# Kernel optimization log

Hardware: AMD Instinct MI355X
Metric: run time of the kernel (lower is better)

Reference implementation:

```python
import jax, jax.numpy as jnp
import numpy as np

VOCAB = 100000
DIM = 256
BATCH = 16384
CTX = 20          # 2 * context_window
NUM_NEG = 5
ALPHA = 0.5
EPS = 1e-6


def setup_inputs() -> dict:
    key = jax.random.key(0)
    k_t, k_c, k_n, k_f, k_wf, k_wr, k_wi = jax.random.split(key, 7)
    # xavier_uniform bound for [VOCAB, DIM] weight
    bound = float(np.sqrt(6.0 / (VOCAB + DIM)))
    return {
        "target_tokens": jax.random.randint(k_t, (BATCH,), 0, VOCAB),
        "context_tokens": jax.random.randint(k_c, (BATCH, CTX), 0, VOCAB),
        "negative_samples": jax.random.randint(k_n, (BATCH, NUM_NEG), 0, VOCAB),
        "token_frequencies": jax.random.uniform(k_f, (VOCAB,), jnp.float32, 1.0, 1000.0),
        "W_fwd": jax.random.uniform(k_wf, (VOCAB, DIM), jnp.float32, -bound, bound),
        "W_rev": jax.random.uniform(k_wr, (VOCAB, DIM), jnp.float32, -bound, bound),
        "W_iso": jax.random.normal(k_wi, (VOCAB, DIM), jnp.float32) * 0.02,
    }


def reference(target_tokens, context_tokens, negative_samples,
              token_frequencies, W_fwd, W_rev, W_iso):
    # blended (orphic) embedding per target token: [B, D]
    contextual = ALPHA * W_fwd[target_tokens] + (1.0 - ALPHA) * W_rev[target_tokens]
    scaling = 1.0 / (1.0 + jnp.log(token_frequencies + EPS))          # [V]
    orphic = contextual + W_iso[target_tokens] * scaling[target_tokens][:, None]

    # positive skip-gram scores: [B, C]
    pos_scores = jnp.einsum('bd,bcd->bc', orphic, W_fwd[context_tokens])
    positive_loss = -jnp.log(jax.nn.sigmoid(pos_scores) + EPS).mean()

    # negative scores: [B, K]; per-sample mean, summed over batch (matches torch loop)
    neg_scores = jnp.einsum('bd,bkd->bk', orphic, W_fwd[negative_samples])
    negative_loss = (-jnp.log(jax.nn.sigmoid(-neg_scores) + EPS)).mean(axis=1).sum()

    return positive_loss + negative_loss
```

## Files before the change

### kernel.cpp

```cpp
#include <hip/hip_runtime.h>
#include <hip/hip_fp8.h>
#include <math.h>

#define VOCAB   100000
#define DIM     256
#define BATCH   16384
#define CTX     20
#define NUM_NEG 5
#define NTOK    (CTX + NUM_NEG)
#define ALPHA   0.5f
#define EPS     1e-6f
#define SCALE     512.0f
#define INV_SCALE (1.0f / 512.0f)

#define WAVES_PER_BLOCK 4
#define NBLOCKS (BATCH / WAVES_PER_BLOCK)

#if __has_builtin(__builtin_amdgcn_cvt_pk_f32_fp8) && __has_builtin(__builtin_amdgcn_cvt_pk_fp8_f32)
#define HW_FP8 1
typedef float v2f __attribute__((ext_vector_type(2)));
#else
#define HW_FP8 0
#endif

__global__ __launch_bounds__(256) void convert_wf(
    const float* __restrict__ Wf, uint4* __restrict__ wf8)
{
    const size_t t = (size_t)blockIdx.x * 256 + threadIdx.x;
    const float4* src = (const float4*)Wf + t * 4;
    float4 a = src[0], b = src[1], c = src[2], d = src[3];
    unsigned int r0, r1, r2, r3;
#if HW_FP8
    r0 = (unsigned)__builtin_amdgcn_cvt_pk_fp8_f32(a.x*SCALE, a.y*SCALE, 0, false);
    r0 = (unsigned)__builtin_amdgcn_cvt_pk_fp8_f32(a.z*SCALE, a.w*SCALE, (int)r0, true);
    r1 = (unsigned)__builtin_amdgcn_cvt_pk_fp8_f32(b.x*SCALE, b.y*SCALE, 0, false);
    r1 = (unsigned)__builtin_amdgcn_cvt_pk_fp8_f32(b.z*SCALE, b.w*SCALE, (int)r1, true);
    r2 = (unsigned)__builtin_amdgcn_cvt_pk_fp8_f32(c.x*SCALE, c.y*SCALE, 0, false);
    r2 = (unsigned)__builtin_amdgcn_cvt_pk_fp8_f32(c.z*SCALE, c.w*SCALE, (int)r2, true);
    r3 = (unsigned)__builtin_amdgcn_cvt_pk_fp8_f32(d.x*SCALE, d.y*SCALE, 0, false);
    r3 = (unsigned)__builtin_amdgcn_cvt_pk_fp8_f32(d.z*SCALE, d.w*SCALE, (int)r3, true);
#else
    {
        const float v[16] = {a.x,a.y,a.z,a.w,b.x,b.y,b.z,b.w,c.x,c.y,c.z,c.w,d.x,d.y,d.z,d.w};
        unsigned int rr[4] = {0,0,0,0};
        for (int i = 0; i < 16; ++i) {
            unsigned int byte = (unsigned int)__hip_cvt_float_to_fp8(v[i]*SCALE, __HIP_SATFINITE, __HIP_E4M3);
            rr[i >> 2] |= byte << ((i & 3) * 8);
        }
        r0 = rr[0]; r1 = rr[1]; r2 = rr[2]; r3 = rr[3];
    }
#endif
    wf8[t] = make_uint4(r0, r1, r2, r3);
}

__device__ __forceinline__ void decode8(unsigned int u, float* e) {
#if HW_FP8
    v2f p0 = __builtin_amdgcn_cvt_pk_f32_fp8((int)u, false);
    v2f p1 = __builtin_amdgcn_cvt_pk_f32_fp8((int)u, true);
    e[0] = p0.x; e[1] = p0.y; e[2] = p1.x; e[3] = p1.y;
#else
    for (int i = 0; i < 4; ++i) {
        __half_raw h = __hip_cvt_fp8_to_halfraw((__hip_fp8_storage_t)((u >> (8*i)) & 0xFF), __HIP_E4M3);
        e[i] = __half2float(__half(h));
    }
#endif
}

__global__ __launch_bounds__(256) void orphic_main_fp8(
    const int*   __restrict__ tgt,
    const int*   __restrict__ ctx,
    const int*   __restrict__ neg,
    const float* __restrict__ freq,
    const float* __restrict__ Wf,
    const float* __restrict__ Wr,
    const float* __restrict__ Wi,
    const uint4* __restrict__ wf8,
    float*       __restrict__ partial)
{
    const int wave = threadIdx.x >> 6;
    const int lane = threadIdx.x & 63;
    const int g    = lane >> 4;
    const int q    = lane & 15;
    const int b    = blockIdx.x * WAVES_PER_BLOCK + wave;

    const int t = tgt[b];
    const float* ft  = Wf + (size_t)t * DIM + q * 16;
    const float* rt  = Wr + (size_t)t * DIM + q * 16;
    const float* it_ = Wi + (size_t)t * DIM + q * 16;
    float o[16];
    {
        float4 f0 = *(const float4*)(ft + 0),  f1 = *(const float4*)(ft + 4);
        float4 f2 = *(const float4*)(ft + 8),  f3 = *(const float4*)(ft + 12);
        float4 r0 = *(const float4*)(rt + 0),  r1 = *(const float4*)(rt + 4);
        float4 r2 = *(const float4*)(rt + 8),  r3 = *(const float4*)(rt + 12);
        float4 w0 = *(const float4*)(it_ + 0), w1 = *(const float4*)(it_ + 4);
        float4 w2 = *(const float4*)(it_ + 8), w3 = *(const float4*)(it_ + 12);
        const float sc = 1.0f / (1.0f + logf(freq[t] + EPS));
        const float ff[16] = {f0.x,f0.y,f0.z,f0.w,f1.x,f1.y,f1.z,f1.w,f2.x,f2.y,f2.z,f2.w,f3.x,f3.y,f3.z,f3.w};
        const float rr[16] = {r0.x,r0.y,r0.z,r0.w,r1.x,r1.y,r1.z,r1.w,r2.x,r2.y,r2.z,r2.w,r3.x,r3.y,r3.z,r3.w};
        const float ww[16] = {w0.x,w0.y,w0.z,w0.w,w1.x,w1.y,w1.z,w1.w,w2.x,w2.y,w2.z,w2.w,w3.x,w3.y,w3.z,w3.w};
        #pragma unroll
        for (int i = 0; i < 16; ++i)
            o[i] = ALPHA * ff[i] + (1.0f - ALPHA) * rr[i] + ww[i] * sc;
    }

    int tok = 0;
    if (lane < CTX)       tok = ctx[(size_t)b * CTX + lane];
    else if (lane < NTOK) tok = neg[(size_t)b * NUM_NEG + (lane - CTX)];

    float posacc = 0.0f, negacc = 0.0f;

    #pragma unroll 2
    for (int it = 0; it < 7; ++it) {
        const int j = it * 4 + g;
        const bool valid = (j < NTOK);
        const int jc = valid ? j : (NTOK - 1);
        const int tj = __shfl(tok, jc, 64);

        const uint4 u = wf8[(size_t)tj * (DIM / 16) + q];
        float e[16];
        decode8(u.x, e + 0);
        decode8(u.y, e + 4);
        decode8(u.z, e + 8);
        decode8(u.w, e + 12);

        float d = 0.0f;
        #pragma unroll
        for (int i = 0; i < 16; ++i) d += o[i] * e[i];

        d += __shfl_xor(d, 1, 64);
        d += __shfl_xor(d, 2, 64);
        d += __shfl_xor(d, 4, 64);
        d += __shfl_xor(d, 8, 64);

        const float s = d * INV_SCALE;
        const float sgn = (jc < CTX) ? -1.0f : 1.0f;
        const float loss = -logf(1.0f / (1.0f + expf(sgn * s)) + EPS);
        if (valid) {
            if (jc < CTX) posacc += loss;
            else          negacc += loss;
        }
    }
    negacc *= (1.0f / NUM_NEG);

    float p = (q == 0) ? posacc : 0.0f;
    float n = (q == 0) ? negacc : 0.0f;
    p += __shfl_xor(p, 16, 64);  p += __shfl_xor(p, 32, 64);
    n += __shfl_xor(n, 16, 64);  n += __shfl_xor(n, 32, 64);

    __shared__ float sp[WAVES_PER_BLOCK];
    __shared__ float sn[WAVES_PER_BLOCK];
    if (lane == 0) { sp[wave] = p; sn[wave] = n; }
    __syncthreads();
    if (threadIdx.x == 0) {
        partial[(size_t)blockIdx.x * 2 + 0] = sp[0] + sp[1] + sp[2] + sp[3];
        partial[(size_t)blockIdx.x * 2 + 1] = sn[0] + sn[1] + sn[2] + sn[3];
    }
}

__global__ __launch_bounds__(256) void orphic_main_f32(
    const int*   __restrict__ tgt,
    const int*   __restrict__ ctx,
    const int*   __restrict__ neg,
    const float* __restrict__ freq,
    const float* __restrict__ Wf,
    const float* __restrict__ Wr,
    const float* __restrict__ Wi,
    float*       __restrict__ partial)
{
    const int wave = threadIdx.x >> 6;
    const int lane = threadIdx.x & 63;
    const int g    = lane >> 4;
    const int q    = lane & 15;
    const int b    = blockIdx.x * WAVES_PER_BLOCK + wave;

    const int t = tgt[b];
    const float* ft  = Wf + (size_t)t * DIM + q * 16;
    const float* rt  = Wr + (size_t)t * DIM + q * 16;
    const float* it_ = Wi + (size_t)t * DIM + q * 16;
    float o[16];
    {
        const float sc = 1.0f / (1.0f + logf(freq[t] + EPS));
        #pragma unroll
        for (int i = 0; i < 16; ++i)
            o[i] = ALPHA * ft[i] + (1.0f - ALPHA) * rt[i] + it_[i] * sc;
    }

    int tok = 0;
    if (lane < CTX)       tok = ctx[(size_t)b * CTX + lane];
    else if (lane < NTOK) tok = neg[(size_t)b * NUM_NEG + (lane - CTX)];

    float posacc = 0.0f, negacc = 0.0f;
    #pragma unroll 2
    for (int it = 0; it < 7; ++it) {
        const int j = it * 4 + g;
        const bool valid = (j < NTOK);
        const int jc = valid ? j : (NTOK - 1);
        const int tj = __shfl(tok, jc, 64);
        const float* e = Wf + (size_t)tj * DIM + q * 16;
        float d = 0.0f;
        #pragma unroll
        for (int i = 0; i < 16; ++i) d += o[i] * e[i];
        d += __shfl_xor(d, 1, 64);
        d += __shfl_xor(d, 2, 64);
        d += __shfl_xor(d, 4, 64);
        d += __shfl_xor(d, 8, 64);
        const float sgn = (jc < CTX) ? -1.0f : 1.0f;
        const float loss = -logf(1.0f / (1.0f + expf(sgn * d)) + EPS);
        if (valid) {
            if (jc < CTX) posacc += loss;
            else          negacc += loss;
        }
    }
    negacc *= (1.0f / NUM_NEG);

    float p = (q == 0) ? posacc : 0.0f;
    float n = (q == 0) ? negacc : 0.0f;
    p += __shfl_xor(p, 16, 64);  p += __shfl_xor(p, 32, 64);
    n += __shfl_xor(n, 16, 64);  n += __shfl_xor(n, 32, 64);

    __shared__ float sp[WAVES_PER_BLOCK];
    __shared__ float sn[WAVES_PER_BLOCK];
    if (lane == 0) { sp[wave] = p; sn[wave] = n; }
    __syncthreads();
    if (threadIdx.x == 0) {
        partial[(size_t)blockIdx.x * 2 + 0] = sp[0] + sp[1] + sp[2] + sp[3];
        partial[(size_t)blockIdx.x * 2 + 1] = sn[0] + sn[1] + sn[2] + sn[3];
    }
}

__global__ __launch_bounds__(256) void orphic_reduce(
    const float* __restrict__ partial, float* __restrict__ out)
{
    double p = 0.0, n = 0.0;
    for (int i = threadIdx.x; i < NBLOCKS; i += 256) {
        p += (double)partial[(size_t)i * 2 + 0];
        n += (double)partial[(size_t)i * 2 + 1];
    }
    __shared__ double lp[256];
    __shared__ double ln[256];
    lp[threadIdx.x] = p;
    ln[threadIdx.x] = n;
    __syncthreads();
    for (int s = 128; s > 0; s >>= 1) {
        if (threadIdx.x < s) {
            lp[threadIdx.x] += lp[threadIdx.x + s];
            ln[threadIdx.x] += ln[threadIdx.x + s];
        }
        __syncthreads();
    }
    if (threadIdx.x == 0) {
        out[0] = (float)(lp[0] / (double)((size_t)BATCH * CTX) + ln[0]);
    }
}

extern "C" void kernel_launch(void* const* d_in, const int* in_sizes, int n_in,
                              void* d_out, int out_size, void* d_ws, size_t ws_size,
                              hipStream_t stream) {
    const int*   tgt  = (const int*)  d_in[0];
    const int*   ctx  = (const int*)  d_in[1];
    const int*   neg  = (const int*)  d_in[2];
    const float* freq = (const float*)d_in[3];
    const float* Wf   = (const float*)d_in[4];
    const float* Wr   = (const float*)d_in[5];
    const float* Wi   = (const float*)d_in[6];
    float* out = (float*)d_out;

    const size_t tbl_bytes = (size_t)VOCAB * DIM;
    const size_t need = tbl_bytes + (size_t)NBLOCKS * 2 * sizeof(float);

    if (ws_size >= need) {
        uint4* wf8 = (uint4*)d_ws;
        float* partial = (float*)((char*)d_ws + tbl_bytes);
        convert_wf<<<VOCAB * DIM / 16 / 256, 256, 0, stream>>>(Wf, wf8);
        orphic_main_fp8<<<NBLOCKS, 256, 0, stream>>>(tgt, ctx, neg, freq, Wf, Wr, Wi, wf8, partial);
        orphic_reduce<<<1, 256, 0, stream>>>(partial, out);
    } else {
        float* partial = (float*)d_ws;
        orphic_main_f32<<<NBLOCKS, 256, 0, stream>>>(tgt, ctx, neg, freq, Wf, Wr, Wi, partial);
        orphic_reduce<<<1, 256, 0, stream>>>(partial, out);
    }
}
```

Before: 53.02 us.

## Merge fp8 table conversion with orphic-row build and batch gather loads in scorer

The fp8 conversion of W_fwd and the computation of the blended orphic rows now run as two block ranges of a single kernel, so the orphic gathers from three fp32 tables overlap with the table conversion. The scoring kernel reads precomputed orphic rows and issues all seven fp8 gathers up front before decoding, which increases memory-level parallelism. In exchange, each 16K×256 fp32 orphic row set is written and then read back through the workspace, and the larger unrolled load set uses more registers.

```diff
diff --git a/kernel.cpp b/kernel.cpp
--- a/kernel.cpp
+++ b/kernel.cpp
@@ -13,8 +13,10 @@
 #define SCALE     512.0f
 #define INV_SCALE (1.0f / 512.0f)
 
-#define WAVES_PER_BLOCK 4
-#define NBLOCKS (BATCH / WAVES_PER_BLOCK)
+#define WPB          4
+#define CONV_BLOCKS  6250
+#define BUILD_BLOCKS (BATCH / WPB)
+#define SCORE_BLOCKS (BATCH / WPB)
 
 #if __has_builtin(__builtin_amdgcn_cvt_pk_f32_fp8) && __has_builtin(__builtin_amdgcn_cvt_pk_fp8_f32)
 #define HW_FP8 1
@@ -23,34 +25,17 @@
 #define HW_FP8 0
 #endif
 
-__global__ __launch_bounds__(256) void convert_wf(
-    const float* __restrict__ Wf, uint4* __restrict__ wf8)
-{
-    const size_t t = (size_t)blockIdx.x * 256 + threadIdx.x;
-    const float4* src = (const float4*)Wf + t * 4;
-    float4 a = src[0], b = src[1], c = src[2], d = src[3];
-    unsigned int r0, r1, r2, r3;
+__device__ __forceinline__ unsigned int pack8(float a, float b, float c, float d) {
 #if HW_FP8
-    r0 = (unsigned)__builtin_amdgcn_cvt_pk_fp8_f32(a.x*SCALE, a.y*SCALE, 0, false);
-    r0 = (unsigned)__builtin_amdgcn_cvt_pk_fp8_f32(a.z*SCALE, a.w*SCALE, (int)r0, true);
-    r1 = (unsigned)__builtin_amdgcn_cvt_pk_fp8_f32(b.x*SCALE, b.y*SCALE, 0, false);
-    r1 = (unsigned)__builtin_amdgcn_cvt_pk_fp8_f32(b.z*SCALE, b.w*SCALE, (int)r1, true);
-    r2 = (unsigned)__builtin_amdgcn_cvt_pk_fp8_f32(c.x*SCALE, c.y*SCALE, 0, false);
-    r2 = (unsigned)__builtin_amdgcn_cvt_pk_fp8_f32(c.z*SCALE, c.w*SCALE, (int)r2, true);
-    r3 = (unsigned)__builtin_amdgcn_cvt_pk_fp8_f32(d.x*SCALE, d.y*SCALE, 0, false);
-    r3 = (unsigned)__builtin_amdgcn_cvt_pk_fp8_f32(d.z*SCALE, d.w*SCALE, (int)r3, true);
+    unsigned int r = (unsigned)__builtin_amdgcn_cvt_pk_fp8_f32(a, b, 0, false);
+    return (unsigned)__builtin_amdgcn_cvt_pk_fp8_f32(c, d, (int)r, true);
 #else
-    {
-        const float v[16] = {a.x,a.y,a.z,a.w,b.x,b.y,b.z,b.w,c.x,c.y,c.z,c.w,d.x,d.y,d.z,d.w};
-        unsigned int rr[4] = {0,0,0,0};
-        for (int i = 0; i < 16; ++i) {
-            unsigned int byte = (unsigned int)__hip_cvt_float_to_fp8(v[i]*SCALE, __HIP_SATFINITE, __HIP_E4M3);
-            rr[i >> 2] |= byte << ((i & 3) * 8);
-        }
-        r0 = rr[0]; r1 = rr[1]; r2 = rr[2]; r3 = rr[3];
-    }
+    const float v[4] = {a, b, c, d};
+    unsigned int r = 0;
+    for (int i = 0; i < 4; ++i)
+        r |= ((unsigned)__hip_cvt_float_to_fp8(v[i], __HIP_SATFINITE, __HIP_E4M3)) << (8 * i);
+    return r;
 #endif
-    wf8[t] = make_uint4(r0, r1, r2, r3);
 }
 
 __device__ __forceinline__ void decode8(unsigned int u, float* e) {
@@ -66,79 +51,99 @@
 #endif
 }
 
-__global__ __launch_bounds__(256) void orphic_main_fp8(
-    const int*   __restrict__ tgt,
-    const int*   __restrict__ ctx,
-    const int*   __restrict__ neg,
-    const float* __restrict__ freq,
+__global__ __launch_bounds__(256) void k1_convert_build(
     const float* __restrict__ Wf,
     const float* __restrict__ Wr,
     const float* __restrict__ Wi,
-    const uint4* __restrict__ wf8,
-    float*       __restrict__ partial)
+    const float* __restrict__ freq,
+    const int*   __restrict__ tgt,
+    uint4*       __restrict__ wf8,
+    float4*      __restrict__ orphic)
+{
+    if (blockIdx.x < CONV_BLOCKS) {
+        const size_t t = (size_t)blockIdx.x * 256 + threadIdx.x;
+        const float4* src = (const float4*)Wf + t * 4;
+        float4 a = src[0], b = src[1], c = src[2], d = src[3];
+        uint4 r;
+        r.x = pack8(a.x*SCALE, a.y*SCALE, a.z*SCALE, a.w*SCALE);
+        r.y = pack8(b.x*SCALE, b.y*SCALE, b.z*SCALE, b.w*SCALE);
+        r.z = pack8(c.x*SCALE, c.y*SCALE, c.z*SCALE, c.w*SCALE);
+        r.w = pack8(d.x*SCALE, d.y*SCALE, d.z*SCALE, d.w*SCALE);
+        wf8[t] = r;
+    } else {
+        const int wave = threadIdx.x >> 6;
+        const int lane = threadIdx.x & 63;
+        const int row  = (blockIdx.x - CONV_BLOCKS) * WPB + wave;
+        const int t    = tgt[row];
+        const float4 f = *(const float4*)(Wf + (size_t)t * DIM + lane * 4);
+        const float4 r = *(const float4*)(Wr + (size_t)t * DIM + lane * 4);
+        const float4 w = *(const float4*)(Wi + (size_t)t * DIM + lane * 4);
+        const float sc = 1.0f / (1.0f + logf(freq[t] + EPS));
+        float4 o;
+        o.x = ALPHA*f.x + (1.0f-ALPHA)*r.x + w.x*sc;
+        o.y = ALPHA*f.y + (1.0f-ALPHA)*r.y + w.y*sc;
+        o.z = ALPHA*f.z + (1.0f-ALPHA)*r.z + w.z*sc;
+        o.w = ALPHA*f.w + (1.0f-ALPHA)*r.w + w.w*sc;
+        orphic[(size_t)row * (DIM/4) + lane] = o;
+    }
+}
+
+__global__ __launch_bounds__(256) void k2_score(
+    const int*    __restrict__ ctx,
+    const int*    __restrict__ neg,
+    const uint4*  __restrict__ wf8,
+    const float4* __restrict__ orphic,
+    float*        __restrict__ partial)
 {
     const int wave = threadIdx.x >> 6;
     const int lane = threadIdx.x & 63;
     const int g    = lane >> 4;
     const int q    = lane & 15;
-    const int b    = blockIdx.x * WAVES_PER_BLOCK + wave;
-
-    const int t = tgt[b];
-    const float* ft  = Wf + (size_t)t * DIM + q * 16;
-    const float* rt  = Wr + (size_t)t * DIM + q * 16;
-    const float* it_ = Wi + (size_t)t * DIM + q * 16;
-    float o[16];
-    {
-        float4 f0 = *(const float4*)(ft + 0),  f1 = *(const float4*)(ft + 4);
-        float4 f2 = *(const float4*)(ft + 8),  f3 = *(const float4*)(ft + 12);
-        float4 r0 = *(const float4*)(rt + 0),  r1 = *(const float4*)(rt + 4);
-        float4 r2 = *(const float4*)(rt + 8),  r3 = *(const float4*)(rt + 12);
-        float4 w0 = *(const float4*)(it_ + 0), w1 = *(const float4*)(it_ + 4);
-        float4 w2 = *(const float4*)(it_ + 8), w3 = *(const float4*)(it_ + 12);
-        const float sc = 1.0f / (1.0f + logf(freq[t] + EPS));
-        const float ff[16] = {f0.x,f0.y,f0.z,f0.w,f1.x,f1.y,f1.z,f1.w,f2.x,f2.y,f2.z,f2.w,f3.x,f3.y,f3.z,f3.w};
-        const float rr[16] = {r0.x,r0.y,r0.z,r0.w,r1.x,r1.y,r1.z,r1.w,r2.x,r2.y,r2.z,r2.w,r3.x,r3.y,r3.z,r3.w};
-        const float ww[16] = {w0.x,w0.y,w0.z,w0.w,w1.x,w1.y,w1.z,w1.w,w2.x,w2.y,w2.z,w2.w,w3.x,w3.y,w3.z,w3.w};
-        #pragma unroll
-        for (int i = 0; i < 16; ++i)
-            o[i] = ALPHA * ff[i] + (1.0f - ALPHA) * rr[i] + ww[i] * sc;
-    }
+    const int b    = blockIdx.x * WPB + wave;
+
+    const float4* orow = orphic + (size_t)b * (DIM/4) + q * 4;
+    const float4 o0 = orow[0], o1 = orow[1], o2 = orow[2], o3 = orow[3];
 
     int tok = 0;
     if (lane < CTX)       tok = ctx[(size_t)b * CTX + lane];
     else if (lane < NTOK) tok = neg[(size_t)b * NUM_NEG + (lane - CTX)];
 
-    float posacc = 0.0f, negacc = 0.0f;
-
-    #pragma unroll 2
+    int jc[7];
+    uint4 u[7];
+    #pragma unroll
     for (int it = 0; it < 7; ++it) {
         const int j = it * 4 + g;
-        const bool valid = (j < NTOK);
-        const int jc = valid ? j : (NTOK - 1);
-        const int tj = __shfl(tok, jc, 64);
-
-        const uint4 u = wf8[(size_t)tj * (DIM / 16) + q];
+        jc[it] = (j < NTOK) ? j : (NTOK - 1);
+        const int tj = __shfl(tok, jc[it], 64);
+        u[it] = wf8[(size_t)tj * (DIM/16) + q];
+    }
+
+    float posacc = 0.0f, negacc = 0.0f;
+    #pragma unroll
+    for (int it = 0; it < 7; ++it) {
         float e[16];
-        decode8(u.x, e + 0);
-        decode8(u.y, e + 4);
-        decode8(u.z, e + 8);
-        decode8(u.w, e + 12);
-
-        float d = 0.0f;
-        #pragma unroll
-        for (int i = 0; i < 16; ++i) d += o[i] * e[i];
+        decode8(u[it].x, e + 0);
+        decode8(u[it].y, e + 4);
+        decode8(u[it].z, e + 8);
+        decode8(u[it].w, e + 12);
+
+        float d = o0.x*e[0]  + o0.y*e[1]  + o0.z*e[2]  + o0.w*e[3]
+                + o1.x*e[4]  + o1.y*e[5]  + o1.z*e[6]  + o1.w*e[7]
+                + o2.x*e[8]  + o2.y*e[9]  + o2.z*e[10] + o2.w*e[11]
+                + o3.x*e[12] + o3.y*e[13] + o3.z*e[14] + o3.w*e[15];
 
         d += __shfl_xor(d, 1, 64);
         d += __shfl_xor(d, 2, 64);
         d += __shfl_xor(d, 4, 64);
         d += __shfl_xor(d, 8, 64);
 
-        const float s = d * INV_SCALE;
-        const float sgn = (jc < CTX) ? -1.0f : 1.0f;
+        const bool valid = (it * 4 + g < NTOK);
+        const float s   = d * INV_SCALE;
+        const float sgn = (jc[it] < CTX) ? -1.0f : 1.0f;
         const float loss = -logf(1.0f / (1.0f + expf(sgn * s)) + EPS);
         if (valid) {
-            if (jc < CTX) posacc += loss;
-            else          negacc += loss;
+            if (jc[it] < CTX) posacc += loss;
+            else              negacc += loss;
         }
     }
     negacc *= (1.0f / NUM_NEG);
@@ -148,8 +153,8 @@
     p += __shfl_xor(p, 16, 64);  p += __shfl_xor(p, 32, 64);
     n += __shfl_xor(n, 16, 64);  n += __shfl_xor(n, 32, 64);
 
-    __shared__ float sp[WAVES_PER_BLOCK];
-    __shared__ float sn[WAVES_PER_BLOCK];
+    __shared__ float sp[WPB];
+    __shared__ float sn[WPB];
     if (lane == 0) { sp[wave] = p; sn[wave] = n; }
     __syncthreads();
     if (threadIdx.x == 0) {
@@ -158,82 +163,11 @@
     }
 }
 
-__global__ __launch_bounds__(256) void orphic_main_f32(
-    const int*   __restrict__ tgt,
-    const int*   __restrict__ ctx,
-    const int*   __restrict__ neg,
-    const float* __restrict__ freq,
-    const float* __restrict__ Wf,
-    const float* __restrict__ Wr,
-    const float* __restrict__ Wi,
-    float*       __restrict__ partial)
-{
-    const int wave = threadIdx.x >> 6;
-    const int lane = threadIdx.x & 63;
-    const int g    = lane >> 4;
-    const int q    = lane & 15;
-    const int b    = blockIdx.x * WAVES_PER_BLOCK + wave;
-
-    const int t = tgt[b];
-    const float* ft  = Wf + (size_t)t * DIM + q * 16;
-    const float* rt  = Wr + (size_t)t * DIM + q * 16;
-    const float* it_ = Wi + (size_t)t * DIM + q * 16;
-    float o[16];
-    {
-        const float sc = 1.0f / (1.0f + logf(freq[t] + EPS));
-        #pragma unroll
-        for (int i = 0; i < 16; ++i)
-            o[i] = ALPHA * ft[i] + (1.0f - ALPHA) * rt[i] + it_[i] * sc;
-    }
-
-    int tok = 0;
-    if (lane < CTX)       tok = ctx[(size_t)b * CTX + lane];
-    else if (lane < NTOK) tok = neg[(size_t)b * NUM_NEG + (lane - CTX)];
-
-    float posacc = 0.0f, negacc = 0.0f;
-    #pragma unroll 2
-    for (int it = 0; it < 7; ++it) {
-        const int j = it * 4 + g;
-        const bool valid = (j < NTOK);
-        const int jc = valid ? j : (NTOK - 1);
-        const int tj = __shfl(tok, jc, 64);
-        const float* e = Wf + (size_t)tj * DIM + q * 16;
-        float d = 0.0f;
-        #pragma unroll
-        for (int i = 0; i < 16; ++i) d += o[i] * e[i];
-        d += __shfl_xor(d, 1, 64);
-        d += __shfl_xor(d, 2, 64);
-        d += __shfl_xor(d, 4, 64);
-        d += __shfl_xor(d, 8, 64);
-        const float sgn = (jc < CTX) ? -1.0f : 1.0f;
-        const float loss = -logf(1.0f / (1.0f + expf(sgn * d)) + EPS);
-        if (valid) {
-            if (jc < CTX) posacc += loss;
-            else          negacc += loss;
-        }
-    }
-    negacc *= (1.0f / NUM_NEG);
-
-    float p = (q == 0) ? posacc : 0.0f;
-    float n = (q == 0) ? negacc : 0.0f;
-    p += __shfl_xor(p, 16, 64);  p += __shfl_xor(p, 32, 64);
-    n += __shfl_xor(n, 16, 64);  n += __shfl_xor(n, 32, 64);
-
-    __shared__ float sp[WAVES_PER_BLOCK];
-    __shared__ float sn[WAVES_PER_BLOCK];
-    if (lane == 0) { sp[wave] = p; sn[wave] = n; }
-    __syncthreads();
-    if (threadIdx.x == 0) {
-        partial[(size_t)blockIdx.x * 2 + 0] = sp[0] + sp[1] + sp[2] + sp[3];
-        partial[(size_t)blockIdx.x * 2 + 1] = sn[0] + sn[1] + sn[2] + sn[3];
-    }
-}
-
 __global__ __launch_bounds__(256) void orphic_reduce(
     const float* __restrict__ partial, float* __restrict__ out)
 {
     double p = 0.0, n = 0.0;
-    for (int i = threadIdx.x; i < NBLOCKS; i += 256) {
+    for (int i = threadIdx.x; i < SCORE_BLOCKS; i += 256) {
         p += (double)partial[(size_t)i * 2 + 0];
         n += (double)partial[(size_t)i * 2 + 1];
     }
@@ -254,6 +188,77 @@
     }
 }
 
+__global__ __launch_bounds__(256) void orphic_main_f32(
+    const int*   __restrict__ tgt,
+    const int*   __restrict__ ctx,
+    const int*   __restrict__ neg,
+    const float* __restrict__ freq,
+    const float* __restrict__ Wf,
+    const float* __restrict__ Wr,
+    const float* __restrict__ Wi,
+    float*       __restrict__ partial)
+{
+    const int wave = threadIdx.x >> 6;
+    const int lane = threadIdx.x & 63;
+    const int g    = lane >> 4;
+    const int q    = lane & 15;
+    const int b    = blockIdx.x * WPB + wave;
+
+    const int t = tgt[b];
+    const float* ft  = Wf + (size_t)t * DIM + q * 16;
+    const float* rt  = Wr + (size_t)t * DIM + q * 16;
+    const float* it_ = Wi + (size_t)t * DIM + q * 16;
+    float o[16];
+    {
+        const float sc = 1.0f / (1.0f + logf(freq[t] + EPS));
+        #pragma unroll
+        for (int i = 0; i < 16; ++i)
+            o[i] = ALPHA * ft[i] + (1.0f - ALPHA) * rt[i] + it_[i] * sc;
+    }
+
+    int tok = 0;
+    if (lane < CTX)       tok = ctx[(size_t)b * CTX + lane];
+    else if (lane < NTOK) tok = neg[(size_t)b * NUM_NEG + (lane - CTX)];
+
+    float posacc = 0.0f, negacc = 0.0f;
+    #pragma unroll 2
+    for (int it = 0; it < 7; ++it) {
+        const int j = it * 4 + g;
+        const bool valid = (j < NTOK);
+        const int jcc = valid ? j : (NTOK - 1);
+        const int tj = __shfl(tok, jcc, 64);
+        const float* e = Wf + (size_t)tj * DIM + q * 16;
+        float d = 0.0f;
+        #pragma unroll
+        for (int i = 0; i < 16; ++i) d += o[i] * e[i];
+        d += __shfl_xor(d, 1, 64);
+        d += __shfl_xor(d, 2, 64);
+        d += __shfl_xor(d, 4, 64);
+        d += __shfl_xor(d, 8, 64);
+        const float sgn = (jcc < CTX) ? -1.0f : 1.0f;
+        const float loss = -logf(1.0f / (1.0f + expf(sgn * d)) + EPS);
+        if (valid) {
+            if (jcc < CTX) posacc += loss;
+            else           negacc += loss;
+        }
+    }
+    negacc *= (1.0f / NUM_NEG);
+
+    float p = (q == 0) ? posacc : 0.0f;
+    float n = (q == 0) ? negacc : 0.0f;
+    p += __shfl_xor(p, 16, 64);  p += __shfl_xor(p, 32, 64);
+    n += __shfl_xor(n, 16, 64);  n += __shfl_xor(n, 32, 64);
+
+    __shared__ float sp[WPB];
+    __shared__ float sn[WPB];
+    if (lane == 0) { sp[wave] = p; sn[wave] = n; }
+    __syncthreads();
+    if (threadIdx.x == 0) {
+        partial[(size_t)blockIdx.x * 2 + 0] = sp[0] + sp[1] + sp[2] + sp[3];
+        partial[(size_t)blockIdx.x * 2 + 1] = sn[0] + sn[1] + sn[2] + sn[3];
+    }
+}
+
 extern "C" void kernel_launch(void* const* d_in, const int* in_sizes, int n_in,
                               void* d_out, int out_size, void* d_ws, size_t ws_size,
                               hipStream_t stream) {
@@ -266,18 +271,21 @@
     const float* Wi   = (const float*)d_in[6];
     float* out = (float*)d_out;
 
-    const size_t tbl_bytes = (size_t)VOCAB * DIM;
-    const size_t need = tbl_bytes + (size_t)NBLOCKS * 2 * sizeof(float);
+    const size_t tbl_bytes  = (size_t)VOCAB * DIM;
+    const size_t orph_bytes = (size_t)BATCH * DIM * sizeof(float);
+    const size_t need = tbl_bytes + orph_bytes + (size_t)SCORE_BLOCKS * 2 * sizeof(float);
 
     if (ws_size >= need) {
-        uint4* wf8 = (uint4*)d_ws;
-        float* partial = (float*)((char*)d_ws + tbl_bytes);
-        convert_wf<<<VOCAB * DIM / 16 / 256, 256, 0, stream>>>(Wf, wf8);
-        orphic_main_fp8<<<NBLOCKS, 256, 0, stream>>>(tgt, ctx, neg, freq, Wf, Wr, Wi, wf8, partial);
+        uint4*  wf8     = (uint4*)d_ws;
+        float4* orphic  = (float4*)((char*)d_ws + tbl_bytes);
+        float*  partial = (float*)((char*)d_ws + tbl_bytes + orph_bytes);
+        k1_convert_build<<<CONV_BLOCKS + BUILD_BLOCKS, 256, 0, stream>>>(
+            Wf, Wr, Wi, freq, tgt, wf8, orphic);
+        k2_score<<<SCORE_BLOCKS, 256, 0, stream>>>(ctx, neg, wf8, orphic, partial);
         orphic_reduce<<<1, 256, 0, stream>>>(partial, out);
     } else {
         float* partial = (float*)d_ws;
-        orphic_main_f32<<<NBLOCKS, 256, 0, stream>>>(tgt, ctx, neg, freq, Wf, Wr, Wi, partial);
+        orphic_main_f32<<<BUILD_BLOCKS, 256, 0, stream>>>(tgt, ctx, neg, freq, Wf, Wr, Wi, partial);
         orphic_reduce<<<1, 256, 0, stream>>>(partial, out);
     }
 }
```

Result: slower. 57.63 us (+8.7%).
